# Kernel tuning notes

Hardware: AMD Instinct MI355X
Metric: run time of the kernel (lower is better)

The kernel has to match this reference:

```python
import jax, jax.numpy as jnp
from jax import lax
import numpy as np

B, C, H, W = 32, 256, 56, 56
G1, G2 = 64, 4          # groups for 3x3 convs, number of parallel convs / 1x1 groups
EPS = 1e-5
DN = ('NCHW', 'OIHW', 'NCHW')


def setup_inputs() -> dict:
    key = jax.random.key(0)
    it = iter(jax.random.split(key, 32))
    nk = lambda: next(it)
    n = lambda shape, s=0.05: jax.random.normal(nk(), shape, jnp.float32) * s
    u = lambda shape: jax.random.uniform(nk(), shape, jnp.float32, minval=0.5, maxval=1.5)
    inp = {'x': jax.random.normal(nk(), (B, C, H, W), jnp.float32)}
    inp.update(
        w1=n((G2, G1, C // G1, 3, 3), 0.1), b1=n((G2, G1)),
        bn1a_g=1.0 + n((C,)), bn1a_b=n((C,)), bn1a_m=n((C,)), bn1a_v=u((C,)),
        pw1=n((C, C // G2, 1, 1), 0.1), pb1=n((C,)),
        bn1b_g=1.0 + n((C,)), bn1b_b=n((C,)), bn1b_m=n((C,)), bn1b_v=u((C,)),
        w2=n((G2, G1, C // G1, 3, 3), 0.1), b2=n((G2, G1)),
        bn2a_g=1.0 + n((C,)), bn2a_b=n((C,)), bn2a_m=n((C,)), bn2a_v=u((C,)),
        pw2=n((C, C // G2, 1, 1), 0.1), pb2=n((C,)),
        bn2b_g=1.0 + n((C,)), bn2b_b=n((C,)), bn2b_m=n((C,)), bn2b_v=u((C,)),
    )
    return inp


def _bn_relu(x, g, b, m, v):
    # inference-mode BatchNorm2d + ReLU, fused into one affine + relu
    inv = g / jnp.sqrt(v + EPS)
    return jax.nn.relu(x * inv[None, :, None, None] + (b - m * inv)[None, :, None, None])


def _gconv3x3(x, w, b):
    # Faithful to: [Conv2d(Cin, g1, k=3, p=1, groups=g1) for _ in range(g2)] then concat(dim=1).
    # Implemented as ONE grouped conv (feature_group_count=g1) followed by a cheap channel permute
    # to recover torch's concat ordering (conv-index major, group minor).
    g2, g1, cpg = w.shape[0], w.shape[1], w.shape[2]
    # combined weight: out channel k*g2 + i (group-major) uses conv i, group k
    Wc = jnp.transpose(w, (1, 0, 2, 3, 4)).reshape(g1 * g2, cpg, 3, 3)
    y = lax.conv_general_dilated(x, Wc, (1, 1), ((1, 1), (1, 1)),
                                 feature_group_count=g1, dimension_numbers=DN)
    Bx, _, Hy, Wy = y.shape
    # (g, i) ordering -> torch concat (i, g) ordering
    y = y.reshape(Bx, g1, g2, Hy, Wy).transpose(0, 2, 1, 3, 4).reshape(Bx, g1 * g2, Hy, Wy)
    return y + b.reshape(g1 * g2)[None, :, None, None]


def _pwconv(x, w, b):
    # Conv2d(C, C, k=1, groups=G2)
    y = lax.conv_general_dilated(x, w, (1, 1), 'VALID',
                                 feature_group_count=G2, dimension_numbers=DN)
    return y + b[None, :, None, None]


def reference(x, w1, b1, bn1a_g, bn1a_b, bn1a_m, bn1a_v, pw1, pb1,
              bn1b_g, bn1b_b, bn1b_m, bn1b_v,
              w2, b2, bn2a_g, bn2a_b, bn2a_m, bn2a_v, pw2, pb2,
              bn2b_g, bn2b_b, bn2b_m, bn2b_v):
    h = _gconv3x3(x, w1, b1)
    h = _bn_relu(h, bn1a_g, bn1a_b, bn1a_m, bn1a_v)
    h = _pwconv(h, pw1, pb1)
    h = _bn_relu(h, bn1b_g, bn1b_b, bn1b_m, bn1b_v)
    h = _gconv3x3(h, w2, b2)
    h = _bn_relu(h, bn2a_g, bn2a_b, bn2a_m, bn2a_v)
    h = _pwconv(h, pw2, pb2)
    h = _bn_relu(h, bn2b_g, bn2b_b, bn2b_m, bn2b_v)
    return h
```

## Files before the change

### kernel.cpp

```cpp
#include <hip/hip_runtime.h>

#define HW 3136
#define SHS 232

__global__ __launch_bounds__(256, 2) void fused_stage(
    const float* __restrict__ in,
    const float* __restrict__ gw,
    const float* __restrict__ gb,
    const float* __restrict__ bnag, const float* __restrict__ bnab,
    const float* __restrict__ bnam, const float* __restrict__ bnav,
    const float* __restrict__ pw,
    const float* __restrict__ pb,
    const float* __restrict__ bnbg, const float* __restrict__ bnbb,
    const float* __restrict__ bnbm, const float* __restrict__ bnbv,
    float* __restrict__ out)
{
    __shared__ float sH[64 * SHS];

    const int tid = threadIdx.x;

    const int idx  = blockIdx.x;
    const int xcd  = idx & 7;
    const int qq   = idx >> 3;
    const int g    = qq & 3;
    const int slot = qq >> 2;
    const int u    = slot * 8 + xcd;
    const int b    = u / 14;
    const int t    = u - b * 14;
    const int y0   = t * 4;

    const int k  = tid >> 2;
    const int xs = tid & 3;
    const int x0 = xs * 14;

    float wr[36];
    {
        const float4* w4 = (const float4*)(gw + (size_t)(g * 64 + k) * 36);
#pragma unroll
        for (int j = 0; j < 9; ++j) {
            float4 v = w4[j];
            wr[4*j+0] = v.x; wr[4*j+1] = v.y; wr[4*j+2] = v.z; wr[4*j+3] = v.w;
        }
    }

    float acc[4][14];
#pragma unroll
    for (int r = 0; r < 4; ++r)
#pragma unroll
        for (int xx = 0; xx < 14; ++xx) acc[r][xx] = 0.f;

#pragma unroll
    for (int cc = 0; cc < 4; ++cc) {
        const float* chp = in + ((size_t)(b * 256 + k * 4 + cc)) * HW;
#pragma unroll
        for (int ry = 0; ry < 6; ++ry) {
            const int gy = y0 - 1 + ry;
            if ((unsigned)gy >= 56u) continue;
            const float* rp = chp + gy * 56;
            float rr[16];
#pragma unroll
            for (int j = 0; j < 7; ++j) {
                float2 v = *(const float2*)(rp + x0 + 2 * j);
                rr[1 + 2*j] = v.x; rr[2 + 2*j] = v.y;
            }
            const float left  = __shfl_up(rr[14], 1);
            const float right = __shfl_down(rr[1], 1);
            rr[0]  = (xs == 0) ? 0.f : left;
            rr[15] = (xs == 3) ? 0.f : right;
            const int rlo = (ry >= 2) ? ry - 2 : 0;
            const int rhi = (ry <= 3) ? ry : 3;
#pragma unroll
            for (int r = 0; r < 4; ++r) {
                if (r < rlo || r > rhi) continue;
                const int dy = ry - r;
                const float w0 = wr[cc*9 + dy*3 + 0];
                const float w1 = wr[cc*9 + dy*3 + 1];
                const float w2 = wr[cc*9 + dy*3 + 2];
#pragma unroll
                for (int xx = 0; xx < 14; ++xx)
                    acc[r][xx] = fmaf(w2, rr[xx+2],
                                 fmaf(w1, rr[xx+1],
                                 fmaf(w0, rr[xx], acc[r][xx])));
            }
        }
    }

    {
        const int c = g * 64 + k;
        const float sc = bnag[c] * rsqrtf(bnav[c] + 1e-5f);
        const float sh = fmaf(gb[c], sc, bnab[c] - bnam[c] * sc);
#pragma unroll
        for (int r = 0; r < 4; ++r)
#pragma unroll
            for (int j = 0; j < 7; ++j) {
                float v0 = fmaxf(fmaf(acc[r][2*j],   sc, sh), 0.f);
                float v1 = fmaxf(fmaf(acc[r][2*j+1], sc, sh), 0.f);
                *(float2*)&sH[k * SHS + r * 56 + x0 + 2*j] = make_float2(v0, v1);
            }
    }
    __syncthreads();

    const int og = tid >> 4;
    const int pg = tid & 15;
    const int p0 = pg * 14;

    float a2[4][14];
#pragma unroll
    for (int i = 0; i < 4; ++i)
#pragma unroll
        for (int xx = 0; xx < 14; ++xx) a2[i][xx] = 0.f;

    const float* wp = pw + (size_t)(g * 64 + og * 4) * 64;

    for (int c4 = 0; c4 < 64; c4 += 4) {
        const float4 wv0 = *(const float4*)(wp + 0 * 64 + c4);
        const float4 wv1 = *(const float4*)(wp + 1 * 64 + c4);
        const float4 wv2 = *(const float4*)(wp + 2 * 64 + c4);
        const float4 wv3 = *(const float4*)(wp + 3 * 64 + c4);
        const float w0a[4] = {wv0.x, wv0.y, wv0.z, wv0.w};
        const float w1a[4] = {wv1.x, wv1.y, wv1.z, wv1.w};
        const float w2a[4] = {wv2.x, wv2.y, wv2.z, wv2.w};
        const float w3a[4] = {wv3.x, wv3.y, wv3.z, wv3.w};
#pragma unroll
        for (int q2 = 0; q2 < 4; ++q2) {
            const float* hrow = &sH[(c4 + q2) * SHS + p0];
            float hr[14];
#pragma unroll
            for (int j = 0; j < 7; ++j) {
                float2 v = *(const float2*)&hrow[2*j];
                hr[2*j] = v.x; hr[2*j+1] = v.y;
            }
            const float wa = w0a[q2], wb = w1a[q2], wc = w2a[q2], wd = w3a[q2];
#pragma unroll
            for (int xx = 0; xx < 14; ++xx) {
                a2[0][xx] = fmaf(wa, hr[xx], a2[0][xx]);
                a2[1][xx] = fmaf(wb, hr[xx], a2[1][xx]);
                a2[2][xx] = fmaf(wc, hr[xx], a2[2][xx]);
                a2[3][xx] = fmaf(wd, hr[xx], a2[3][xx]);
            }
        }
    }

#pragma unroll
    for (int i = 0; i < 4; ++i) {
        const int o = g * 64 + og * 4 + i;
        const float sc = bnbg[o] * rsqrtf(bnbv[o] + 1e-5f);
        const float sh = fmaf(pb[o], sc, bnbb[o] - bnbm[o] * sc);
        float* op = out + ((size_t)(b * 256 + o)) * HW + y0 * 56 + p0;
#pragma unroll
        for (int j = 0; j < 7; ++j) {
            float v0 = fmaxf(fmaf(a2[i][2*j],   sc, sh), 0.f);
            float v1 = fmaxf(fmaf(a2[i][2*j+1], sc, sh), 0.f);
            *(float2*)(op + 2*j) = make_float2(v0, v1);
        }
    }
}

extern "C" void kernel_launch(void* const* d_in, const int* in_sizes, int n_in,
                              void* d_out, int out_size, void* d_ws, size_t ws_size,
                              hipStream_t stream) {
    const float* x     = (const float*)d_in[0];
    const float* w1    = (const float*)d_in[1];
    const float* b1    = (const float*)d_in[2];
    const float* bn1ag = (const float*)d_in[3];
    const float* bn1ab = (const float*)d_in[4];
    const float* bn1am = (const float*)d_in[5];
    const float* bn1av = (const float*)d_in[6];
    const float* pw1   = (const float*)d_in[7];
    const float* pb1   = (const float*)d_in[8];
    const float* bn1bg = (const float*)d_in[9];
    const float* bn1bb = (const float*)d_in[10];
    const float* bn1bm = (const float*)d_in[11];
    const float* bn1bv = (const float*)d_in[12];
    const float* w2    = (const float*)d_in[13];
    const float* b2    = (const float*)d_in[14];
    const float* bn2ag = (const float*)d_in[15];
    const float* bn2ab = (const float*)d_in[16];
    const float* bn2am = (const float*)d_in[17];
    const float* bn2av = (const float*)d_in[18];
    const float* pw2   = (const float*)d_in[19];
    const float* pb2   = (const float*)d_in[20];
    const float* bn2bg = (const float*)d_in[21];
    const float* bn2bb = (const float*)d_in[22];
    const float* bn2bm = (const float*)d_in[23];
    const float* bn2bv = (const float*)d_in[24];

    float* mid  = (float*)d_ws;
    float* outp = (float*)d_out;

    const int grid = 32 * 4 * 14;

    fused_stage<<<grid, 256, 0, stream>>>(x,   w1, b1, bn1ag, bn1ab, bn1am, bn1av,
                                          pw1, pb1, bn1bg, bn1bb, bn1bm, bn1bv, mid);
    fused_stage<<<grid, 256, 0, stream>>>(mid, w2, b2, bn2ag, bn2ab, bn2am, bn2av,
                                          pw2, pb2, bn2bg, bn2bb, bn2bm, bn2bv, outp);
}
```

Measured before the change: 417.4 us.

## Split fused stage into separate grouped 3x3 conv and pointwise conv kernels

Replaces the per-stage fused kernel with two kernels. The first is a grouped 3x3 conv plus BN/ReLU, where each wave handles one channel over a 14-row strip using lane shuffles for horizontal neighbours, with higher occupancy (launch bounds 8). The second is a pointwise grouped conv that loads tiles into shared memory. This is meant to cut the redundant halo row reads and the register pressure of the fused kernel. In exchange, each stage writes and reads back a full intermediate activation tensor in global memory. The final pointwise pass works in place on the output buffer.

```diff
diff --git a/kernel.cpp b/kernel.cpp
--- a/kernel.cpp
+++ b/kernel.cpp
@@ -3,100 +3,104 @@
 #define HW 3136
 #define SHS 232
 
-__global__ __launch_bounds__(256, 2) void fused_stage(
+__global__ __launch_bounds__(256, 8) void gconv3(
     const float* __restrict__ in,
     const float* __restrict__ gw,
     const float* __restrict__ gb,
-    const float* __restrict__ bnag, const float* __restrict__ bnab,
-    const float* __restrict__ bnam, const float* __restrict__ bnav,
+    const float* __restrict__ bng, const float* __restrict__ bnb,
+    const float* __restrict__ bnm, const float* __restrict__ bnv,
+    float* __restrict__ h)
+{
+    const int idx   = blockIdx.x;
+    const int xcd   = idx & 7;
+    const int i     = xcd & 3;
+    const int kcl   = xcd >> 2;
+    const int rest  = idx >> 3;
+    const int b     = rest >> 5;
+    const int r2    = rest & 31;
+    const int strip = r2 >> 3;
+    const int kch   = r2 & 7;
+    const int kc    = kch * 2 + kcl;
+
+    const int l  = threadIdx.x & 63;
+    const int wv = threadIdx.x >> 6;
+    const int k  = __builtin_amdgcn_readfirstlane(kc * 4 + wv);
+    const int ys = strip * 14;
+
+    const int cmid = i * 64 + k;
+    const float* wk = gw + (size_t)cmid * 36;
+
+    float acc[14];
+#pragma unroll
+    for (int r = 0; r < 14; ++r) acc[r] = 0.f;
+
+    const float* chp0 = in + ((size_t)(b * 256 + k * 4)) * HW;
+
+#pragma unroll
+    for (int cc = 0; cc < 4; ++cc) {
+        const float w00 = wk[cc*9+0], w01 = wk[cc*9+1], w02 = wk[cc*9+2];
+        const float w10 = wk[cc*9+3], w11 = wk[cc*9+4], w12 = wk[cc*9+5];
+        const float w20 = wk[cc*9+6], w21 = wk[cc*9+7], w22 = wk[cc*9+8];
+        const float* chp = chp0 + cc * HW;
+#pragma unroll
+        for (int ry = 0; ry < 16; ++ry) {
+            const int gy = ys - 1 + ry;
+            float v = 0.f;
+            if ((unsigned)gy < 56u && l < 56) v = chp[gy * 56 + l];
+            const float Ls = __shfl_up(v, 1);
+            const float R  = __shfl_down(v, 1);
+            const float L  = (l == 0) ? 0.f : Ls;
+#pragma unroll
+            for (int dy = 0; dy < 3; ++dy) {
+                const int orr = ry - dy;
+                if (orr < 0 || orr > 13) continue;
+                const float wa = (dy == 0) ? w00 : (dy == 1) ? w10 : w20;
+                const float wb = (dy == 0) ? w01 : (dy == 1) ? w11 : w21;
+                const float wc = (dy == 0) ? w02 : (dy == 1) ? w12 : w22;
+                acc[orr] = fmaf(wc, R, fmaf(wb, v, fmaf(wa, L, acc[orr])));
+            }
+        }
+    }
+
+    const float sc = bng[cmid] * rsqrtf(bnv[cmid] + 1e-5f);
+    const float sh = fmaf(gb[cmid], sc, bnb[cmid] - bnm[cmid] * sc);
+    if (l < 56) {
+        float* op = h + ((size_t)(b * 256 + cmid)) * HW + ys * 56 + l;
+#pragma unroll
+        for (int r = 0; r < 14; ++r)
+            op[r * 56] = fmaxf(fmaf(acc[r], sc, sh), 0.f);
+    }
+}
+
+__global__ __launch_bounds__(256, 2) void pconv(
+    const float* __restrict__ h,
     const float* __restrict__ pw,
     const float* __restrict__ pb,
-    const float* __restrict__ bnbg, const float* __restrict__ bnbb,
-    const float* __restrict__ bnbm, const float* __restrict__ bnbv,
+    const float* __restrict__ bng, const float* __restrict__ bnb,
+    const float* __restrict__ bnm, const float* __restrict__ bnv,
     float* __restrict__ out)
 {
-    __shared__ float sH[64 * SHS];
-
-    const int tid = threadIdx.x;
-
-    const int idx  = blockIdx.x;
-    const int xcd  = idx & 7;
-    const int qq   = idx >> 3;
-    const int g    = qq & 3;
-    const int slot = qq >> 2;
-    const int u    = slot * 8 + xcd;
-    const int b    = u / 14;
-    const int t    = u - b * 14;
-    const int y0   = t * 4;
-
-    const int k  = tid >> 2;
-    const int xs = tid & 3;
-    const int x0 = xs * 14;
-
-    float wr[36];
+    __shared__ float sHt[64 * SHS];
+
+    const int blk  = blockIdx.x;
+    const int b    = blk / 56;
+    const int rem  = blk - b * 56;
+    const int g    = rem / 14;
+    const int tile = rem - g * 14;
+    const int pxb  = tile * 224;
+    const int tid  = threadIdx.x;
+
     {
-        const float4* w4 = (const float4*)(gw + (size_t)(g * 64 + k) * 36);
-#pragma unroll
-        for (int j = 0; j < 9; ++j) {
-            float4 v = w4[j];
-            wr[4*j+0] = v.x; wr[4*j+1] = v.y; wr[4*j+2] = v.z; wr[4*j+3] = v.w;
-        }
-    }
-
-    float acc[4][14];
-#pragma unroll
-    for (int r = 0; r < 4; ++r)
-#pragma unroll
-        for (int xx = 0; xx < 14; ++xx) acc[r][xx] = 0.f;
-
-#pragma unroll
-    for (int cc = 0; cc < 4; ++cc) {
-        const float* chp = in + ((size_t)(b * 256 + k * 4 + cc)) * HW;
-#pragma unroll
-        for (int ry = 0; ry < 6; ++ry) {
-            const int gy = y0 - 1 + ry;
-            if ((unsigned)gy >= 56u) continue;
-            const float* rp = chp + gy * 56;
-            float rr[16];
-#pragma unroll
-            for (int j = 0; j < 7; ++j) {
-                float2 v = *(const float2*)(rp + x0 + 2 * j);
-                rr[1 + 2*j] = v.x; rr[2 + 2*j] = v.y;
-            }
-            const float left  = __shfl_up(rr[14], 1);
-            const float right = __shfl_down(rr[1], 1);
-            rr[0]  = (xs == 0) ? 0.f : left;
-            rr[15] = (xs == 3) ? 0.f : right;
-            const int rlo = (ry >= 2) ? ry - 2 : 0;
-            const int rhi = (ry <= 3) ? ry : 3;
-#pragma unroll
-            for (int r = 0; r < 4; ++r) {
-                if (r < rlo || r > rhi) continue;
-                const int dy = ry - r;
-                const float w0 = wr[cc*9 + dy*3 + 0];
-                const float w1 = wr[cc*9 + dy*3 + 1];
-                const float w2 = wr[cc*9 + dy*3 + 2];
-#pragma unroll
-                for (int xx = 0; xx < 14; ++xx)
-                    acc[r][xx] = fmaf(w2, rr[xx+2],
-                                 fmaf(w1, rr[xx+1],
-                                 fmaf(w0, rr[xx], acc[r][xx])));
-            }
-        }
-    }
-
-    {
-        const int c = g * 64 + k;
-        const float sc = bnag[c] * rsqrtf(bnav[c] + 1e-5f);
-        const float sh = fmaf(gb[c], sc, bnab[c] - bnam[c] * sc);
-#pragma unroll
-        for (int r = 0; r < 4; ++r)
-#pragma unroll
-            for (int j = 0; j < 7; ++j) {
-                float v0 = fmaxf(fmaf(acc[r][2*j],   sc, sh), 0.f);
-                float v1 = fmaxf(fmaf(acc[r][2*j+1], sc, sh), 0.f);
-                *(float2*)&sH[k * SHS + r * 56 + x0 + 2*j] = make_float2(v0, v1);
-            }
+        int c   = tid / 56;
+        int px4 = tid - c * 56;
+        const float* base = h + ((size_t)(b * 256 + g * 64)) * HW + pxb;
+#pragma unroll
+        for (int it = 0; it < 14; ++it) {
+            const float4 v = *(const float4*)(base + (size_t)c * HW + px4 * 4);
+            *(float4*)&sHt[c * SHS + px4 * 4] = v;
+            c += 4; px4 += 32;
+            if (px4 >= 56) { px4 -= 56; c += 1; }
+        }
     }
     __syncthreads();
 
@@ -123,11 +127,11 @@
         const float w3a[4] = {wv3.x, wv3.y, wv3.z, wv3.w};
 #pragma unroll
         for (int q2 = 0; q2 < 4; ++q2) {
-            const float* hrow = &sH[(c4 + q2) * SHS + p0];
+            const float* hrow = &sHt[(c4 + q2) * SHS + p0];
             float hr[14];
 #pragma unroll
             for (int j = 0; j < 7; ++j) {
-                float2 v = *(const float2*)&hrow[2*j];
+                float2 v = *(const float2*)&hrow[2 * j];
                 hr[2*j] = v.x; hr[2*j+1] = v.y;
             }
             const float wa = w0a[q2], wb = w1a[q2], wc = w2a[q2], wd = w3a[q2];
@@ -144,9 +148,9 @@
 #pragma unroll
     for (int i = 0; i < 4; ++i) {
         const int o = g * 64 + og * 4 + i;
-        const float sc = bnbg[o] * rsqrtf(bnbv[o] + 1e-5f);
-        const float sh = fmaf(pb[o], sc, bnbb[o] - bnbm[o] * sc);
-        float* op = out + ((size_t)(b * 256 + o)) * HW + y0 * 56 + p0;
+        const float sc = bng[o] * rsqrtf(bnv[o] + 1e-5f);
+        const float sh = fmaf(pb[o], sc, bnb[o] - bnm[o] * sc);
+        float* op = out + ((size_t)(b * 256 + o)) * HW + pxb + p0;
 #pragma unroll
         for (int j = 0; j < 7; ++j) {
             float v0 = fmaxf(fmaf(a2[i][2*j],   sc, sh), 0.f);
@@ -188,10 +192,11 @@
     float* mid  = (float*)d_ws;
     float* outp = (float*)d_out;
 
-    const int grid = 32 * 4 * 14;
-
-    fused_stage<<<grid, 256, 0, stream>>>(x,   w1, b1, bn1ag, bn1ab, bn1am, bn1av,
-                                          pw1, pb1, bn1bg, bn1bb, bn1bm, bn1bv, mid);
-    fused_stage<<<grid, 256, 0, stream>>>(mid, w2, b2, bn2ag, bn2ab, bn2am, bn2av,
-                                          pw2, pb2, bn2bg, bn2bb, bn2bm, bn2bv, outp);
+    const int gridA = 8192;
+    const int gridB = 1792;
+
+    gconv3<<<gridA, 256, 0, stream>>>(x, w1, b1, bn1ag, bn1ab, bn1am, bn1av, outp);
+    pconv <<<gridB, 256, 0, stream>>>(outp, pw1, pb1, bn1bg, bn1bb, bn1bm, bn1bv, mid);
+    gconv3<<<gridA, 256, 0, stream>>>(mid, w2, b2, bn2ag, bn2ab, bn2am, bn2av, outp);
+    pconv <<<gridB, 256, 0, stream>>>(outp, pw2, pb2, bn2bg, bn2bb, bn2bm, bn2bv, outp);
 }
```

Result: slower. 1.555 ms (+272.4%).
